# Kernel optimization log

Measured on AMD Instinct MI355X. Metric: run time of the kernel, lower is better.

## Reference

```python
import jax, jax.numpy as jnp
import numpy as np

M, N_ATOMS, E_MOL, IN_CH, OUT_CH = 10000, 32, 64, 64, 128
HID = 2 * OUT_CH  # 256
E_KG = 320000


def gcn_conv(x, edge_index, W, b):
    # PyG GCNConv: out = D^-1/2 (A+I) D^-1/2 (x W) + b
    N = x.shape[0]
    loops = jnp.arange(N)
    src = jnp.concatenate([edge_index[0], loops])
    dst = jnp.concatenate([edge_index[1], loops])
    deg = jax.ops.segment_sum(jnp.ones_like(dst, dtype=x.dtype), dst, num_segments=N)
    dinv = jnp.where(deg > 0, jax.lax.rsqrt(deg), 0.0)
    norm = dinv[src] * dinv[dst]  # [E+N]
    xw = x @ W  # [N, F_out]
    out = jax.ops.segment_sum(xw[src] * norm[:, None], dst, num_segments=N)
    return out + b


def mol_gnn(mx, mei, W1, b1, W2, b2, W3, b3):
    h = jax.nn.relu(gcn_conv(mx, mei, W1, b1))
    h = jax.nn.relu(gcn_conv(h, mei, W2, b2))
    h = gcn_conv(h, mei, W3, b3)
    return jnp.min(h, axis=0)  # torch.min(dim=0).values


def _glorot(key, shape):
    fan_in, fan_out = shape
    s = jnp.sqrt(6.0 / (fan_in + fan_out))
    return jax.random.uniform(key, shape, jnp.float32, -s, s)


def setup_inputs() -> dict:
    key = jax.random.key(0)
    ks = jax.random.split(key, 16)
    mol_x = jax.random.normal(ks[0], (M, N_ATOMS, IN_CH), jnp.float32)
    mol_edge_index = jax.random.randint(ks[1], (M, 2, E_MOL), 0, N_ATOMS, jnp.int64)
    kg_edge_index = jax.random.randint(ks[2], (2, E_KG), 0, M, jnp.int64)
    return {
        "mol_x": mol_x,
        "mol_edge_index": mol_edge_index,
        "kg_edge_index": kg_edge_index,
        "W1": _glorot(ks[3], (IN_CH, HID)), "b1": jnp.zeros((HID,), jnp.float32),
        "W2": _glorot(ks[4], (HID, HID)), "b2": jnp.zeros((HID,), jnp.float32),
        "W3": _glorot(ks[5], (HID, OUT_CH)), "b3": jnp.zeros((OUT_CH,), jnp.float32),
        "Wk1": _glorot(ks[6], (OUT_CH, HID)), "bk1": jnp.zeros((HID,), jnp.float32),
        "Wk2": _glorot(ks[7], (HID, OUT_CH)), "bk2": jnp.zeros((OUT_CH,), jnp.float32),
    }


def reference(mol_x, mol_edge_index, kg_edge_index, W1, b1, W2, b2, W3, b3, Wk1, bk1, Wk2, bk2):
    # Per-molecule GNN + min-pool, vectorized over the M molecules (each graph is disjoint,
    # so vmap == the original per-graph Python loop)
    embed = jax.vmap(mol_gnn, in_axes=(0, 0, None, None, None, None, None, None))(
        mol_x, mol_edge_index, W1, b1, W2, b2, W3, b3)  # [M, OUT_CH]
    h = jax.nn.relu(gcn_conv(embed, kg_edge_index, Wk1, bk1))
    return gcn_conv(h, kg_edge_index, Wk2, bk2)  # [M, OUT_CH]
```

## Files before the change

kernel.cpp:

```cpp
#include <hip/hip_runtime.h>

#define M_MOLS  10000
#define NA      32
#define E_MOL   64
#define IN_CH   64
#define OUT_CH  128
#define HID     256
#define E_KG    320000
#define KG_N    10000

typedef __attribute__((ext_vector_type(8))) short  s16x8;
typedef __attribute__((ext_vector_type(4))) short  s16x4;
typedef __attribute__((ext_vector_type(4))) float  f32x4;

static __device__ __forceinline__ short f2bf(float f) {
    unsigned u = __float_as_uint(f);
    u += 0x7FFFu + ((u >> 16) & 1u);
    return (short)(u >> 16);
}

__global__ void prep_wt(const float* __restrict__ W, short* __restrict__ WT,
                        int K, int C, int total) {
    int idx = blockIdx.x * 256 + threadIdx.x;
    if (idx < total) {
        int c = idx / K, k = idx - c * K;
        WT[idx] = f2bf(W[k * C + c]);
    }
}

__global__ __launch_bounds__(256, 4) void mol_kernel(
    const float* __restrict__ mol_x, const int* __restrict__ mol_ei,
    const short* __restrict__ WT1, const float* __restrict__ b1,
    const short* __restrict__ WT2, const float* __restrict__ b2,
    const short* __restrict__ WT3, const float* __restrict__ b3,
    const float* __restrict__ dinvk, float* __restrict__ embed)
{
    __shared__ short Hs[NA * HID];
    __shared__ short BT[NA * 40];
    __shared__ float BmT[NA * NA];
    __shared__ float bias_s[2 * HID + OUT_CH];
    __shared__ int   se[E_MOL], de[E_MOL];
    __shared__ float dinv[NA];
    __shared__ int   deg[NA];

    const int t    = threadIdx.x;
    const int mol  = blockIdx.x;
    const int lane = t & 63;
    const int wid  = t >> 6;
    const int lr   = lane & 15;
    const int lk   = lane >> 4;
    char* HsB = (char*)Hs;

    {
        const float4* src = (const float4*)(mol_x + (size_t)mol * (NA * IN_CH));
        float4 a = src[t * 2], b = src[t * 2 + 1];
        s16x8 v;
        v[0] = f2bf(a.x); v[1] = f2bf(a.y); v[2] = f2bf(a.z); v[3] = f2bf(a.w);
        v[4] = f2bf(b.x); v[5] = f2bf(b.y); v[6] = f2bf(b.z); v[7] = f2bf(b.w);
        int row = t >> 3, k0 = (t & 7) * 8;
        int byte = (row << 9) + (k0 << 1); byte ^= (row & 7) << 4;
        *(s16x8*)(HsB + byte) = v;
    }
    {
        const int* eb = mol_ei + (size_t)mol * (2 * E_MOL);
        if (t < E_MOL)            se[t]         = eb[t];
        else if (t < 2 * E_MOL)   de[t - E_MOL] = eb[t];
    }
    if (t < NA) deg[t] = 1;
    for (int i = t; i < NA * NA; i += 256) BmT[i] = 0.f;
    for (int i = t; i < 2 * HID + OUT_CH; i += 256)
        bias_s[i] = (i < HID) ? b1[i] : (i < 2 * HID) ? b2[i - HID] : b3[i - 2 * HID];
    __syncthreads();
    if (t < E_MOL) atomicAdd(&deg[de[t]], 1);
    __syncthreads();
    if (t < NA) dinv[t] = rsqrtf((float)deg[t]);
    __syncthreads();
    if (t < E_MOL) {
        atomicAdd(&BmT[de[t] * NA + se[t]], dinv[se[t]] * dinv[de[t]]);
    } else if (t < E_MOL + NA) {
        int i = t - E_MOL;
        atomicAdd(&BmT[i * NA + i], dinv[i] * dinv[i]);
    }
    __syncthreads();
    for (int i = t; i < NA * NA; i += 256)
        BT[(i >> 5) * 40 + (i & 31)] = f2bf(BmT[i]);
    __syncthreads();

    const f32x4 z4 = {0.f, 0.f, 0.f, 0.f};

#define GEMM_PHASE(WT, K, NCT, CT0)                                            \
    _Pragma("unroll")                                                          \
    for (int it = 0; it < 2; ++it)                                             \
        _Pragma("unroll")                                                      \
        for (int c = 0; c < NCT; ++c) acc[it][c] = z4;                         \
    for (int ks = 0; ks < (K) / 32; ++ks) {                                    \
        s16x8 af[2];                                                           \
        _Pragma("unroll")                                                      \
        for (int it = 0; it < 2; ++it) {                                       \
            int row = it * 16 + lr;                                            \
            int byte = (row << 9) + ((ks * 32 + lk * 8) << 1);                 \
            byte ^= (row & 7) << 4;                                            \
            af[it] = *(const s16x8*)(HsB + byte);                              \
        }                                                                      \
        _Pragma("unroll")                                                      \
        for (int c = 0; c < NCT; ++c) {                                        \
            s16x8 bf = *(const s16x8*)((WT) +                                  \
                (size_t)(((CT0) + c) * 16 + lr) * (K) + ks * 32 + lk * 8);     \
            acc[0][c] = __builtin_amdgcn_mfma_f32_16x16x32_bf16(af[0], bf,     \
                                                               acc[0][c], 0, 0, 0); \
            acc[1][c] = __builtin_amdgcn_mfma_f32_16x16x32_bf16(af[1], bf,     \
                                                               acc[1][c], 0, 0, 0); \
        }                                                                      \
    }

#define TRANSPOSE(cIdx, atf)                                                   \
    {                                                                          \
        float vals[8];                                                         \
        _Pragma("unroll")                                                      \
        for (int m = 0; m < 8; ++m) {                                          \
            int src = ((((lk & 1) << 1) + (m >> 2)) << 4) + lr;                \
            float v0 = __shfl(acc[0][cIdx][m & 3], src);                       \
            float v1 = __shfl(acc[1][cIdx][m & 3], src);                       \
            vals[m] = (lk & 2) ? v1 : v0;                                      \
        }                                                                      \
        _Pragma("unroll")                                                      \
        for (int m = 0; m < 8; ++m) atf[m] = f2bf(vals[m]);                    \
    }

#define AGG_PHASE(NCT, CT0, BOFF, RELU)                                        \
    _Pragma("unroll")                                                          \
    for (int c = 0; c < NCT; ++c) {                                            \
        s16x8 atf;                                                             \
        TRANSPOSE(c, atf)                                                      \
        _Pragma("unroll")                                                      \
        for (int itn = 0; itn < 2; ++itn) {                                    \
            s16x8 btf = *(const s16x8*)(BT + (itn * 16 + lr) * 40 + lk * 8);   \
            f32x4 g = __builtin_amdgcn_mfma_f32_16x16x32_bf16(atf, btf, z4,    \
                                                              0, 0, 0);        \
            int c0 = ((CT0) + c) * 16 + lk * 4;                                \
            s16x4 w;                                                           \
            _Pragma("unroll")                                                  \
            for (int jj = 0; jj < 4; ++jj) {                                   \
                float v = g[jj] + bias_s[(BOFF) + c0 + jj];                    \
                if (RELU) v = v > 0.f ? v : 0.f;                               \
                w[jj] = f2bf(v);                                               \
            }                                                                  \
            int row = itn * 16 + lr;                                           \
            int byte = (row << 9) + (c0 << 1); byte ^= (row & 7) << 4;         \
            *(s16x4*)(HsB + byte) = w;                                         \
        }                                                                      \
    }

    const int ct0 = wid * 4;
    const int ct3 = wid * 2;
    {
        f32x4 acc[2][4];
        GEMM_PHASE(WT1, IN_CH, 4, ct0)
        __syncthreads();
        AGG_PHASE(4, ct0, 0, true)
        __syncthreads();
    }
    {
        f32x4 acc[2][4];
        GEMM_PHASE(WT2, HID, 4, ct0)
        __syncthreads();
        AGG_PHASE(4, ct0, HID, true)
        __syncthreads();
    }
    {
        f32x4 acc[2][2];
        GEMM_PHASE(WT3, HID, 2, ct3)
        __syncthreads();
        #pragma unroll
        for (int c = 0; c < 2; ++c) {
            s16x8 atf;
            TRANSPOSE(c, atf)
            float mn[4] = {1e30f, 1e30f, 1e30f, 1e30f};
            #pragma unroll
            for (int itn = 0; itn < 2; ++itn) {
                s16x8 btf = *(const s16x8*)(BT + (itn * 16 + lr) * 40 + lk * 8);
                f32x4 g = __builtin_amdgcn_mfma_f32_16x16x32_bf16(atf, btf, z4,
                                                                  0, 0, 0);
                #pragma unroll
                for (int jj = 0; jj < 4; ++jj) mn[jj] = fminf(mn[jj], g[jj]);
            }
            #pragma unroll
            for (int off = 1; off < 16; off <<= 1) {
                #pragma unroll
                for (int jj = 0; jj < 4; ++jj)
                    mn[jj] = fminf(mn[jj], __shfl_xor(mn[jj], off));
            }
            if (lr == 0) {
                int c0 = (ct3 + c) * 16 + lk * 4;
                #pragma unroll
                for (int jj = 0; jj < 4; ++jj)
                    BmT[c0 + jj] = mn[jj] + bias_s[2 * HID + c0 + jj];
            }
        }
    }
    __syncthreads();
    if (t < OUT_CH) embed[(size_t)mol * OUT_CH + t] = BmT[t] * dinvk[mol];
#undef GEMM_PHASE
#undef TRANSPOSE
#undef AGG_PHASE
}

__global__ void kg_count(const int* __restrict__ kg_ei, int* __restrict__ degi) {
    int e = blockIdx.x * 256 + threadIdx.x;
    if (e < E_KG) atomicAdd(&degi[kg_ei[E_KG + e]], 1);
}

__global__ void kg_dinv(const int* __restrict__ degi, float* __restrict__ dinvk) {
    int i = blockIdx.x * 256 + threadIdx.x;
    if (i < KG_N) dinvk[i] = rsqrtf((float)(degi[i] + 1));
}

__global__ __launch_bounds__(1024) void scan_kernel(const int* __restrict__ degi,
                                                    int* __restrict__ ptr, int n) {
    __shared__ int wsum[16];
    const int t = threadIdx.x;
    const int base = t * 10;
    int inc[10];
    int s = 0;
    #pragma unroll
    for (int i = 0; i < 10; ++i) {
        int idx = base + i;
        s += (idx < n) ? degi[idx] : 0;
        inc[i] = s;
    }
    const int lane = t & 63;
    int ps = s;
    #pragma unroll
    for (int off = 1; off < 64; off <<= 1) {
        int u = __shfl_up(ps, off);
        if (lane >= off) ps += u;
    }
    if (lane == 63) wsum[t >> 6] = ps;
    __syncthreads();
    if (t == 0) {
        int run = 0;
        #pragma unroll
        for (int k = 0; k < 16; ++k) { int x = wsum[k]; wsum[k] = run; run += x; }
        ptr[0] = 0;
    }
    __syncthreads();
    const int excl = wsum[t >> 6] + (ps - s);
    #pragma unroll
    for (int i = 0; i < 10; ++i) {
        int idx = base + i;
        if (idx < n) ptr[idx + 1] = excl + inc[i];
    }
}

__global__ void kg_fill(const int* __restrict__ kg_ei, const int* __restrict__ ptr,
                        int* __restrict__ cursor, int* __restrict__ csr) {
    int e = blockIdx.x * 256 + threadIdx.x;
    if (e < E_KG) {
        int s = kg_ei[e];
        int d = kg_ei[E_KG + e];
        int pos = atomicAdd(&cursor[d], 1);
        csr[ptr[d] + pos] = s;
    }
}

template <bool ADD_BIAS>
__global__ __launch_bounds__(64) void kg_gather(
    const float* __restrict__ xs, const float* __restrict__ dinvk,
    const int* __restrict__ ptr, const int* __restrict__ csr,
    const float* __restrict__ bias, float* __restrict__ out)
{
    const int sub = threadIdx.x >> 5;
    const int t   = threadIdx.x & 31;
    const int n   = blockIdx.x * 2 + sub;
    const float4* x4 = (const float4*)xs;
    const int e1 = ptr[n + 1];
    float4 acc = x4[(size_t)n * 32 + t];
    for (int e = ptr[n]; e < e1; ++e) {
        int s = csr[e];
        float4 v = x4[(size_t)s * 32 + t];
        acc.x += v.x; acc.y += v.y; acc.z += v.z; acc.w += v.w;
    }
    const float dn = dinvk[n];
    float4 o;
    if (ADD_BIAS) {
        const float4 b = ((const float4*)bias)[t];
        o.x = fmaf(dn, acc.x, b.x); o.y = fmaf(dn, acc.y, b.y);
        o.z = fmaf(dn, acc.z, b.z); o.w = fmaf(dn, acc.w, b.w);
    } else {
        o.x = dn * acc.x; o.y = dn * acc.y; o.z = dn * acc.z; o.w = dn * acc.w;
    }
    ((float4*)out)[(size_t)n * 32 + t] = o;
}

__global__ __launch_bounds__(256) void kg_gemm_relu(const float* __restrict__ X,
                                                    const float* __restrict__ W,
                                                    const float* __restrict__ bias,
                                                    float* __restrict__ Y) {
    __shared__ float es[4 * OUT_CH];
    const int t  = threadIdx.x;
    const int r0 = blockIdx.x * 4;
    if (t < 128) ((float4*)es)[t] = ((const float4*)(X + (size_t)r0 * OUT_CH))[t];
    __syncthreads();
    const int c = t;
    float a0 = 0.f, a1 = 0.f, a2 = 0.f, a3 = 0.f;
    for (int k = 0; k < OUT_CH; k += 4) {
        const float w0 = W[(k + 0) * HID + c], w1 = W[(k + 1) * HID + c],
                    w2 = W[(k + 2) * HID + c], w3 = W[(k + 3) * HID + c];
        float4 e0 = *(const float4*)&es[0 * OUT_CH + k];
        float4 e1 = *(const float4*)&es[1 * OUT_CH + k];
        float4 e2 = *(const float4*)&es[2 * OUT_CH + k];
        float4 e3 = *(const float4*)&es[3 * OUT_CH + k];
        a0 = fmaf(e0.x, w0, fmaf(e0.y, w1, fmaf(e0.z, w2, fmaf(e0.w, w3, a0))));
        a1 = fmaf(e1.x, w0, fmaf(e1.y, w1, fmaf(e1.z, w2, fmaf(e1.w, w3, a1))));
        a2 = fmaf(e2.x, w0, fmaf(e2.y, w1, fmaf(e2.z, w2, fmaf(e2.w, w3, a2))));
        a3 = fmaf(e3.x, w0, fmaf(e3.y, w1, fmaf(e3.z, w2, fmaf(e3.w, w3, a3))));
    }
    const float bc = bias[c];
    float v0 = a0 + bc, v1 = a1 + bc, v2 = a2 + bc, v3 = a3 + bc;
    Y[(size_t)(r0 + 0) * HID + c] = v0 > 0.f ? v0 : 0.f;
    Y[(size_t)(r0 + 1) * HID + c] = v1 > 0.f ? v1 : 0.f;
    Y[(size_t)(r0 + 2) * HID + c] = v2 > 0.f ? v2 : 0.f;
    Y[(size_t)(r0 + 3) * HID + c] = v3 > 0.f ? v3 : 0.f;
}

__global__ __launch_bounds__(256) void kg_gemm_scale(const float* __restrict__ X,
                                                     const float* __restrict__ W,
                                                     const float* __restrict__ dinvk,
                                                     float* __restrict__ Y) {
    __shared__ float es[8 * HID];
    const int t  = threadIdx.x;
    const int r0 = blockIdx.x * 8;
    {
        const float4* src = (const float4*)(X + (size_t)r0 * HID);
        float4* dst = (float4*)es;
        dst[t]       = src[t];
        dst[t + 256] = src[t + 256];
    }
    __syncthreads();
    const int c   = t & 127;
    const int rr0 = (t >> 7) * 4;
    float acc[4] = {0.f, 0.f, 0.f, 0.f};
    for (int k = 0; k < HID; k += 4) {
        const float w0 = W[(k + 0) * OUT_CH + c], w1 = W[(k + 1) * OUT_CH + c],
                    w2 = W[(k + 2) * OUT_CH + c], w3 = W[(k + 3) * OUT_CH + c];
        #pragma unroll
        for (int r = 0; r < 4; ++r) {
            float4 e = *(const float4*)&es[(rr0 + r) * HID + k];
            acc[r] = fmaf(e.x, w0, fmaf(e.y, w1, fmaf(e.z, w2, fmaf(e.w, w3, acc[r]))));
        }
    }
    #pragma unroll
    for (int r = 0; r < 4; ++r)
        Y[(size_t)(r0 + rr0 + r) * OUT_CH + c] = dinvk[r0 + rr0 + r] * acc[r];
}

extern "C" void kernel_launch(void* const* d_in, const int* in_sizes, int n_in,
                              void* d_out, int out_size, void* d_ws, size_t ws_size,
                              hipStream_t stream) {
    const float* mol_x  = (const float*)d_in[0];
    const int*   mol_ei = (const int*)  d_in[1];
    const int*   kg_ei  = (const int*)  d_in[2];
    const float* W1 = (const float*)d_in[3];  const float* b1 = (const float*)d_in[4];
    const float* W2 = (const float*)d_in[5];  const float* b2 = (const float*)d_in[6];
    const float* W3 = (const float*)d_in[7];  const float* b3 = (const float*)d_in[8];
    const float* Wk1 = (const float*)d_in[9];  const float* bk1 = (const float*)d_in[10];
    const float* Wk2 = (const float*)d_in[11]; const float* bk2 = (const float*)d_in[12];
    float* out = (float*)d_out;

    char* ws = (char*)d_ws;
    size_t off = 0;
    auto alloc = [&](size_t bytes) -> void* {
        void* p = ws + off;
        off += (bytes + 255) & ~(size_t)255;
        return p;
    };
    float* embed = (float*)alloc((size_t)M_MOLS * OUT_CH * 4);
    float* G     = (float*)alloc((size_t)KG_N * OUT_CH * 4);
    float* h1    = (float*)alloc((size_t)KG_N * HID * 4);
    float* xw2s  = (float*)alloc((size_t)KG_N * OUT_CH * 4);
    int*   degi  = (int*)  alloc((size_t)KG_N * 4);
    float* dinvk = (float*)alloc((size_t)KG_N * 4);
    int*   ptr   = (int*)  alloc((size_t)(KG_N + 4) * 4);
    int*   cursor= (int*)  alloc((size_t)KG_N * 4);
    int*   csr   = (int*)  alloc((size_t)E_KG * 4);
    short* wt1   = (short*)alloc((size_t)IN_CH * HID * 2);
    short* wt2   = (short*)alloc((size_t)HID * HID * 2);
    short* wt3   = (short*)alloc((size_t)OUT_CH * HID * 2);

    hipMemsetAsync(degi,   0, (size_t)KG_N * 4, stream);
    hipMemsetAsync(cursor, 0, (size_t)KG_N * 4, stream);

    kg_count<<<(E_KG + 255) / 256, 256, 0, stream>>>(kg_ei, degi);
    scan_kernel<<<1, 1024, 0, stream>>>(degi, ptr, KG_N);
    kg_dinv<<<(KG_N + 255) / 256, 256, 0, stream>>>(degi, dinvk);
    kg_fill<<<(E_KG + 255) / 256, 256, 0, stream>>>(kg_ei, ptr, cursor, csr);

    prep_wt<<<(IN_CH * HID + 255) / 256, 256, 0, stream>>>(W1, wt1, IN_CH, HID, IN_CH * HID);
    prep_wt<<<(HID * HID + 255) / 256, 256, 0, stream>>>(W2, wt2, HID, HID, HID * HID);
    prep_wt<<<(OUT_CH * HID + 255) / 256, 256, 0, stream>>>(W3, wt3, HID, OUT_CH, HID * OUT_CH);

    mol_kernel<<<M_MOLS, 256, 0, stream>>>(mol_x, mol_ei, wt1, b1, wt2, b2, wt3, b3,
                                           dinvk, embed);

    kg_gather<false><<<KG_N / 2, 64, 0, stream>>>(embed, dinvk, ptr, csr, nullptr, G);
    kg_gemm_relu<<<KG_N / 4, 256, 0, stream>>>(G, Wk1, bk1, h1);

    kg_gemm_scale<<<KG_N / 8, 256, 0, stream>>>(h1, Wk2, dinvk, xw2s);
    kg_gather<true><<<KG_N / 2, 64, 0, stream>>>(xw2s, dinvk, ptr, csr, bk2, out);
}
```

Measured before the change: 555.2 us.

## Use packed bf16 converts, bpermute transpose, single-wave setup, fused dinv, unrolled gathers

Replaces the software float-to-bf16 rounding with the hardware v_cvt_pk_bf16_f32 instruction and rewrites the accumulator transpose to permute packed bf16 pairs with ds_bpermute instead of per-element float shuffles. The per-molecule adjacency setup moves into a single wave that uses waitcnt instead of several block barriers, while a second wave loads the biases in parallel, and one __syncthreads before the final aggregation is removed. The kg_dinv kernel is folded into the scan kernel, the CSR gather loop is unrolled by four, and the KG GEMM loops get unroll pragmas. Dropping the barrier and relying on intra-wave ordering for the LDS atomics carries a correctness risk.

```diff
diff --git a/kernel.cpp b/kernel.cpp
--- a/kernel.cpp
+++ b/kernel.cpp
@@ -10,7 +10,6 @@
 #define KG_N    10000
 
 typedef __attribute__((ext_vector_type(8))) short  s16x8;
-typedef __attribute__((ext_vector_type(4))) short  s16x4;
 typedef __attribute__((ext_vector_type(4))) float  f32x4;
 
 static __device__ __forceinline__ short f2bf(float f) {
@@ -18,6 +17,8 @@
     u += 0x7FFFu + ((u >> 16) & 1u);
     return (short)(u >> 16);
 }
+#define CVTPK(dst, lo, hi) \
+    asm("v_cvt_pk_bf16_f32 %0, %1, %2" : "=v"(dst) : "v"(lo), "v"(hi))
 
 __global__ void prep_wt(const float* __restrict__ W, short* __restrict__ WT,
                         int K, int C, int total) {
@@ -39,9 +40,8 @@
     __shared__ short BT[NA * 40];
     __shared__ float BmT[NA * NA];
     __shared__ float bias_s[2 * HID + OUT_CH];
-    __shared__ int   se[E_MOL], de[E_MOL];
     __shared__ float dinv[NA];
-    __shared__ int   deg[NA];
+    __shared__ int   ideg[NA];
 
     const int t    = threadIdx.x;
     const int mol  = blockIdx.x;
@@ -51,39 +51,48 @@
     const int lk   = lane >> 4;
     char* HsB = (char*)Hs;
 
+    const int addrA = ((((lane >> 4) & 1) << 5) + lr) << 2;
+    const int addrB = addrA + 64;
+
     {
         const float4* src = (const float4*)(mol_x + (size_t)mol * (NA * IN_CH));
         float4 a = src[t * 2], b = src[t * 2 + 1];
-        s16x8 v;
-        v[0] = f2bf(a.x); v[1] = f2bf(a.y); v[2] = f2bf(a.z); v[3] = f2bf(a.w);
-        v[4] = f2bf(b.x); v[5] = f2bf(b.y); v[6] = f2bf(b.z); v[7] = f2bf(b.w);
+        int4 v;
+        CVTPK(v.x, a.x, a.y); CVTPK(v.y, a.z, a.w);
+        CVTPK(v.z, b.x, b.y); CVTPK(v.w, b.z, b.w);
         int row = t >> 3, k0 = (t & 7) * 8;
         int byte = (row << 9) + (k0 << 1); byte ^= (row & 7) << 4;
-        *(s16x8*)(HsB + byte) = v;
-    }
-    {
+        *(int4*)(HsB + byte) = v;
+    }
+    if (wid == 0) {
+        float4 z = {0.f, 0.f, 0.f, 0.f};
+        float4* B4 = (float4*)BmT;
+        B4[lane] = z; B4[lane + 64] = z; B4[lane + 128] = z; B4[lane + 192] = z;
         const int* eb = mol_ei + (size_t)mol * (2 * E_MOL);
-        if (t < E_MOL)            se[t]         = eb[t];
-        else if (t < 2 * E_MOL)   de[t - E_MOL] = eb[t];
-    }
-    if (t < NA) deg[t] = 1;
-    for (int i = t; i < NA * NA; i += 256) BmT[i] = 0.f;
-    for (int i = t; i < 2 * HID + OUT_CH; i += 256)
-        bias_s[i] = (i < HID) ? b1[i] : (i < 2 * HID) ? b2[i - HID] : b3[i - 2 * HID];
-    __syncthreads();
-    if (t < E_MOL) atomicAdd(&deg[de[t]], 1);
-    __syncthreads();
-    if (t < NA) dinv[t] = rsqrtf((float)deg[t]);
-    __syncthreads();
-    if (t < E_MOL) {
-        atomicAdd(&BmT[de[t] * NA + se[t]], dinv[se[t]] * dinv[de[t]]);
-    } else if (t < E_MOL + NA) {
-        int i = t - E_MOL;
-        atomicAdd(&BmT[i * NA + i], dinv[i] * dinv[i]);
-    }
-    __syncthreads();
-    for (int i = t; i < NA * NA; i += 256)
-        BT[(i >> 5) * 40 + (i & 31)] = f2bf(BmT[i]);
+        int es_ = eb[lane], ed_ = eb[E_MOL + lane];
+        if (lane < NA) ideg[lane] = 1;
+        asm volatile("s_waitcnt lgkmcnt(0)" ::: "memory");
+        atomicAdd(&ideg[ed_], 1);
+        asm volatile("s_waitcnt lgkmcnt(0)" ::: "memory");
+        if (lane < NA) dinv[lane] = rsqrtf((float)ideg[lane]);
+        asm volatile("s_waitcnt lgkmcnt(0)" ::: "memory");
+        atomicAdd(&BmT[ed_ * NA + es_], dinv[es_] * dinv[ed_]);
+        if (lane < NA) atomicAdd(&BmT[lane * NA + lane], dinv[lane] * dinv[lane]);
+        asm volatile("s_waitcnt lgkmcnt(0)" ::: "memory");
+        int i0 = lane >> 1, s0 = (lane & 1) * 16;
+        #pragma unroll
+        for (int j = 0; j < 4; ++j) {
+            float4 f = *(const float4*)&BmT[i0 * NA + s0 + j * 4];
+            int2 w;
+            CVTPK(w.x, f.x, f.y); CVTPK(w.y, f.z, f.w);
+            *(int2*)&BT[i0 * 40 + s0 + j * 4] = w;
+        }
+    } else if (wid == 1) {
+        float4* d = (float4*)bias_s;
+        d[lane]      = ((const float4*)b1)[lane];
+        d[64 + lane] = ((const float4*)b2)[lane];
+        if (lane < 32) d[128 + lane] = ((const float4*)b3)[lane];
+    }
     __syncthreads();
 
     const f32x4 z4 = {0.f, 0.f, 0.f, 0.f};
@@ -93,6 +102,7 @@
     for (int it = 0; it < 2; ++it)                                             \
         _Pragma("unroll")                                                      \
         for (int c = 0; c < NCT; ++c) acc[it][c] = z4;                         \
+    _Pragma("unroll 2")                                                        \
     for (int ks = 0; ks < (K) / 32; ++ks) {                                    \
         s16x8 af[2];                                                           \
         _Pragma("unroll")                                                      \
@@ -113,41 +123,52 @@
         }                                                                      \
     }
 
-#define TRANSPOSE(cIdx, atf)                                                   \
+#define TRANSPOSE_PK(cIdx, atf)                                                \
     {                                                                          \
-        float vals[8];                                                         \
-        _Pragma("unroll")                                                      \
-        for (int m = 0; m < 8; ++m) {                                          \
-            int src = ((((lk & 1) << 1) + (m >> 2)) << 4) + lr;                \
-            float v0 = __shfl(acc[0][cIdx][m & 3], src);                       \
-            float v1 = __shfl(acc[1][cIdx][m & 3], src);                       \
-            vals[m] = (lk & 2) ? v1 : v0;                                      \
-        }                                                                      \
-        _Pragma("unroll")                                                      \
-        for (int m = 0; m < 8; ++m) atf[m] = f2bf(vals[m]);                    \
+        int pk0A, pk1A, pk0B, pk1B;                                            \
+        CVTPK(pk0A, acc[0][cIdx][0], acc[0][cIdx][1]);                         \
+        CVTPK(pk1A, acc[0][cIdx][2], acc[0][cIdx][3]);                         \
+        CVTPK(pk0B, acc[1][cIdx][0], acc[1][cIdx][1]);                         \
+        CVTPK(pk1B, acc[1][cIdx][2], acc[1][cIdx][3]);                         \
+        int d0A = __builtin_amdgcn_ds_bpermute(addrA, pk0A);                   \
+        int d1A = __builtin_amdgcn_ds_bpermute(addrA, pk1A);                   \
+        int d2A = __builtin_amdgcn_ds_bpermute(addrB, pk0A);                   \
+        int d3A = __builtin_amdgcn_ds_bpermute(addrB, pk1A);                   \
+        int d0B = __builtin_amdgcn_ds_bpermute(addrA, pk0B);                   \
+        int d1B = __builtin_amdgcn_ds_bpermute(addrA, pk1B);                   \
+        int d2B = __builtin_amdgcn_ds_bpermute(addrB, pk0B);                   \
+        int d3B = __builtin_amdgcn_ds_bpermute(addrB, pk1B);                   \
+        bool hi_ = (lk & 2);                                                   \
+        union { int i[4]; s16x8 v; } u_;                                       \
+        u_.i[0] = hi_ ? d0B : d0A; u_.i[1] = hi_ ? d1B : d1A;                  \
+        u_.i[2] = hi_ ? d2B : d2A; u_.i[3] = hi_ ? d3B : d3A;                  \
+        atf = u_.v;                                                            \
     }
 
 #define AGG_PHASE(NCT, CT0, BOFF, RELU)                                        \
     _Pragma("unroll")                                                          \
     for (int c = 0; c < NCT; ++c) {                                            \
         s16x8 atf;                                                             \
-        TRANSPOSE(c, atf)                                                      \
+        TRANSPOSE_PK(c, atf)                                                   \
         _Pragma("unroll")                                                      \
         for (int itn = 0; itn < 2; ++itn) {                                    \
             s16x8 btf = *(const s16x8*)(BT + (itn * 16 + lr) * 40 + lk * 8);   \
             f32x4 g = __builtin_amdgcn_mfma_f32_16x16x32_bf16(atf, btf, z4,    \
                                                               0, 0, 0);        \
             int c0 = ((CT0) + c) * 16 + lk * 4;                                \
-            s16x4 w;                                                           \
-            _Pragma("unroll")                                                  \
-            for (int jj = 0; jj < 4; ++jj) {                                   \
-                float v = g[jj] + bias_s[(BOFF) + c0 + jj];                    \
-                if (RELU) v = v > 0.f ? v : 0.f;                               \
-                w[jj] = f2bf(v);                                               \
+            float v0 = g[0] + bias_s[(BOFF) + c0 + 0];                         \
+            float v1 = g[1] + bias_s[(BOFF) + c0 + 1];                         \
+            float v2 = g[2] + bias_s[(BOFF) + c0 + 2];                         \
+            float v3 = g[3] + bias_s[(BOFF) + c0 + 3];                         \
+            if (RELU) {                                                        \
+                v0 = fmaxf(v0, 0.f); v1 = fmaxf(v1, 0.f);                      \
+                v2 = fmaxf(v2, 0.f); v3 = fmaxf(v3, 0.f);                      \
             }                                                                  \
+            int2 w_;                                                           \
+            CVTPK(w_.x, v0, v1); CVTPK(w_.y, v2, v3);                          \
             int row = itn * 16 + lr;                                           \
             int byte = (row << 9) + (c0 << 1); byte ^= (row & 7) << 4;         \
-            *(s16x4*)(HsB + byte) = w;                                         \
+            *(int2*)(HsB + byte) = w_;                                         \
         }                                                                      \
     }
 
@@ -170,11 +191,10 @@
     {
         f32x4 acc[2][2];
         GEMM_PHASE(WT3, HID, 2, ct3)
-        __syncthreads();
         #pragma unroll
         for (int c = 0; c < 2; ++c) {
             s16x8 atf;
-            TRANSPOSE(c, atf)
+            TRANSPOSE_PK(c, atf)
             float mn[4] = {1e30f, 1e30f, 1e30f, 1e30f};
             #pragma unroll
             for (int itn = 0; itn < 2; ++itn) {
@@ -201,7 +221,7 @@
     __syncthreads();
     if (t < OUT_CH) embed[(size_t)mol * OUT_CH + t] = BmT[t] * dinvk[mol];
 #undef GEMM_PHASE
-#undef TRANSPOSE
+#undef TRANSPOSE_PK
 #undef AGG_PHASE
 }
 
@@ -210,13 +230,9 @@
     if (e < E_KG) atomicAdd(&degi[kg_ei[E_KG + e]], 1);
 }
 
-__global__ void kg_dinv(const int* __restrict__ degi, float* __restrict__ dinvk) {
-    int i = blockIdx.x * 256 + threadIdx.x;
-    if (i < KG_N) dinvk[i] = rsqrtf((float)(degi[i] + 1));
-}
-
 __global__ __launch_bounds__(1024) void scan_kernel(const int* __restrict__ degi,
-                                                    int* __restrict__ ptr, int n) {
+                                                    int* __restrict__ ptr,
+                                                    float* __restrict__ dinvk, int n) {
     __shared__ int wsum[16];
     const int t = threadIdx.x;
     const int base = t * 10;
@@ -225,7 +241,9 @@
     #pragma unroll
     for (int i = 0; i < 10; ++i) {
         int idx = base + i;
-        s += (idx < n) ? degi[idx] : 0;
+        int d = (idx < n) ? degi[idx] : 0;
+        if (idx < n) dinvk[idx] = rsqrtf((float)(d + 1));
+        s += d;
         inc[i] = s;
     }
     const int lane = t & 63;
@@ -273,9 +291,19 @@
     const int t   = threadIdx.x & 31;
     const int n   = blockIdx.x * 2 + sub;
     const float4* x4 = (const float4*)xs;
+    int e = ptr[n];
     const int e1 = ptr[n + 1];
     float4 acc = x4[(size_t)n * 32 + t];
-    for (int e = ptr[n]; e < e1; ++e) {
+    for (; e + 4 <= e1; e += 4) {
+        int s0 = csr[e], s1 = csr[e + 1], s2 = csr[e + 2], s3 = csr[e + 3];
+        float4 v0 = x4[(size_t)s0 * 32 + t], v1 = x4[(size_t)s1 * 32 + t];
+        float4 v2 = x4[(size_t)s2 * 32 + t], v3 = x4[(size_t)s3 * 32 + t];
+        acc.x += v0.x + v1.x + v2.x + v3.x;
+        acc.y += v0.y + v1.y + v2.y + v3.y;
+        acc.z += v0.z + v1.z + v2.z + v3.z;
+        acc.w += v0.w + v1.w + v2.w + v3.w;
+    }
+    for (; e < e1; ++e) {
         int s = csr[e];
         float4 v = x4[(size_t)s * 32 + t];
         acc.x += v.x; acc.y += v.y; acc.z += v.z; acc.w += v.w;
@@ -303,6 +331,7 @@
     __syncthreads();
     const int c = t;
     float a0 = 0.f, a1 = 0.f, a2 = 0.f, a3 = 0.f;
+    #pragma unroll 4
     for (int k = 0; k < OUT_CH; k += 4) {
         const float w0 = W[(k + 0) * HID + c], w1 = W[(k + 1) * HID + c],
                     w2 = W[(k + 2) * HID + c], w3 = W[(k + 3) * HID + c];
@@ -340,6 +369,7 @@
     const int c   = t & 127;
     const int rr0 = (t >> 7) * 4;
     float acc[4] = {0.f, 0.f, 0.f, 0.f};
+    #pragma unroll 4
     for (int k = 0; k < HID; k += 4) {
         const float w0 = W[(k + 0) * OUT_CH + c], w1 = W[(k + 1) * OUT_CH + c],
                     w2 = W[(k + 2) * OUT_CH + c], w3 = W[(k + 3) * OUT_CH + c];
@@ -391,8 +421,7 @@
     hipMemsetAsync(cursor, 0, (size_t)KG_N * 4, stream);
 
     kg_count<<<(E_KG + 255) / 256, 256, 0, stream>>>(kg_ei, degi);
-    scan_kernel<<<1, 1024, 0, stream>>>(degi, ptr, KG_N);
-    kg_dinv<<<(KG_N + 255) / 256, 256, 0, stream>>>(degi, dinvk);
+    scan_kernel<<<1, 1024, 0, stream>>>(degi, ptr, dinvk, KG_N);
     kg_fill<<<(E_KG + 255) / 256, 256, 0, stream>>>(kg_ei, ptr, cursor, csr);
 
     prep_wt<<<(IN_CH * HID + 255) / 256, 256, 0, stream>>>(W1, wt1, IN_CH, HID, IN_CH * HID);
```

Measured after the change: 511.1 us. -7.9%, faster.
